# Optimization experiments

Hardware: AMD Instinct MI355X
Metric: run time of the kernel (lower is better)

Reference implementation:

```python
import jax, jax.numpy as jnp
import numpy as np

S, B, E, H = 2048, 64, 256, 256

def setup_inputs() -> dict:
    key = jax.random.key(0)
    k1, k2, k3, k4, k5 = jax.random.split(key, 5)
    scale = 1.0 / np.sqrt(H)
    return {
        "sentence": jax.random.normal(k1, (S, B, E), dtype=jnp.float32),
        "h0": jax.random.uniform(k2, (B, H), dtype=jnp.float32),
        "W_ih": jax.random.normal(k3, (E, H), dtype=jnp.float32) * scale,
        "W_hh": jax.random.normal(k4, (H, H), dtype=jnp.float32) * scale,
        "b": jax.random.normal(k5, (H,), dtype=jnp.float32) * scale,
    }

def reference(sentence, h0, W_ih, W_hh, b):
    # Precompute input projections for all steps in one big GEMM: [S,B,H]
    x_proj = jnp.einsum("sbe,eh->sbh", sentence, W_ih) + b

    def step(h, xp):
        h_new = jnp.tanh(xp + h @ W_hh)  # [B,H]
        return h_new, None

    h_final, _ = jax.lax.scan(step, h0, x_proj)
    return h_final  # [B,H]
```

## Files before the change

kernel.cpp:

```cpp
#include <hip/hip_runtime.h>
#include <math.h>

#define S_TOT 2048
#define B_    64
#define E_    256
#define H_    256

typedef __fp16 half2v __attribute__((ext_vector_type(2)));

__global__ __launch_bounds__(256, 1) void fused_step(
    const float* __restrict__ A,
    const float* __restrict__ Wih,
    const float* __restrict__ bias,
    float*       __restrict__ xp_next,
    const float* __restrict__ xp_cur,
    const float* __restrict__ Whh,
    float*       __restrict__ h,
    int steps, int scan_blocks)
{
    __shared__ float smem[32 * 68 + 32 * 64];
    const int tid = threadIdx.x;

    if ((int)blockIdx.x < scan_blocks) {
        float* hbuf = smem;
        const int b  = blockIdx.x;
        const int ks = tid & 7;
        const int jg = tid >> 3;
        const int j0 = jg << 3;
        const int jf = j0 + ((ks & 1) << 2) + (ks & 2) + ((ks >> 2) & 1);

        half2v w[16][8];
        #pragma unroll
        for (int i = 0; i < 16; i++) {
            const float* r0 = &Whh[(size_t)(ks * 32 + 2 * i) * H_ + j0];
            const float* r1 = r0 + H_;
            #pragma unroll
            for (int jj = 0; jj < 8; jj++) {
                half2v v = __builtin_amdgcn_cvt_pkrtz(r0[jj], r1[jj]);
                int vi = __builtin_bit_cast(int, v);
                asm volatile("" : "+v"(vi));
                w[i][jj] = __builtin_bit_cast(half2v, vi);
            }
        }

        if (tid < 128) {
            half2v hp = __builtin_amdgcn_cvt_pkrtz(h[b * H_ + 2 * tid],
                                                   h[b * H_ + 2 * tid + 1]);
            const int j = 2 * tid;
            ((half2v*)hbuf)[(j >> 5) * 20 + ((j & 31) >> 1)] = hp;
        }
        float xpn = xp_cur[(size_t)b * H_ + jf];
        __syncthreads();

        int p = 0;
        for (int s = 0; s < steps; s++) {
            const float xpc = xpn;
            if (s + 1 < steps)
                xpn = xp_cur[((size_t)(s + 1) * B_ + b) * H_ + jf];

            half2v hk[16];
            {
                const float4* hs = (const float4*)&hbuf[p * 160 + ks * 20];
                float4 t0 = hs[0], t1 = hs[1], t2 = hs[2], t3 = hs[3];
                *(float4*)&hk[0]  = t0;
                *(float4*)&hk[4]  = t1;
                *(float4*)&hk[8]  = t2;
                *(float4*)&hk[12] = t3;
            }

            float acc[8] = {0.f, 0.f, 0.f, 0.f, 0.f, 0.f, 0.f, 0.f};
            #pragma unroll
            for (int i = 0; i < 16; i++) {
                #pragma unroll
                for (int jj = 0; jj < 8; jj++)
                    acc[jj] = __builtin_amdgcn_fdot2(hk[i], w[i][jj],
                                                     acc[jj], false);
            }

            const bool b0 = (ks & 1), b1 = (ks & 2), b2 = (ks & 4);
            float r0, r1, r2, r3, q0, q1, v;
            {
                float s0 = b0 ? acc[0] : acc[4];
                float s1 = b0 ? acc[1] : acc[5];
                float s2 = b0 ? acc[2] : acc[6];
                float s3 = b0 ? acc[3] : acc[7];
                r0 = (b0 ? acc[4] : acc[0]) + __shfl_xor(s0, 1);
                r1 = (b0 ? acc[5] : acc[1]) + __shfl_xor(s1, 1);
                r2 = (b0 ? acc[6] : acc[2]) + __shfl_xor(s2, 1);
                r3 = (b0 ? acc[7] : acc[3]) + __shfl_xor(s3, 1);
            }
            {
                float s0 = b1 ? r0 : r2;
                float s1 = b1 ? r1 : r3;
                q0 = (b1 ? r2 : r0) + __shfl_xor(s0, 2);
                q1 = (b1 ? r3 : r1) + __shfl_xor(s1, 2);
            }
            {
                float s0 = b2 ? q0 : q1;
                v = (b2 ? q1 : q0) + __shfl_xor(s0, 4);
            }

            v += xpc;
            const float e2 = __expf(2.f * v);
            const float hn = 1.f - 2.f / (e2 + 1.f);
            ((__fp16*)hbuf)[((p ^ 1) * 160 + (jf >> 5) * 20) * 2 + (jf & 31)]
                = (__fp16)hn;
            if (s == steps - 1) h[b * H_ + jf] = hn;
            __syncthreads();
            p ^= 1;
        }
    } else if (A != nullptr) {
        float (*As)[68] = (float(*)[68])smem;
        float (*Bs)[64] = (float(*)[64])(smem + 32 * 68);

        const int gid = blockIdx.x - scan_blocks;
        const int bm = (gid >> 2) * 64;
        const int bn = (gid & 3) * 64;
        const int tx = tid & 15;
        const int ty = tid >> 4;

        float acc[4][4] = {};

        const int ar = tid >> 3;
        const int ak = (tid & 7) << 2;
        const int br = tid >> 4;
        const int bc = (tid & 15) << 2;

        for (int k0 = 0; k0 < E_; k0 += 32) {
            float4 a0 = *(const float4*)&A[(size_t)(bm + ar)      * E_ + k0 + ak];
            float4 a1 = *(const float4*)&A[(size_t)(bm + ar + 32) * E_ + k0 + ak];
            float4 bv0 = *(const float4*)&Wih[(size_t)(k0 + br)      * H_ + bn + bc];
            float4 bv1 = *(const float4*)&Wih[(size_t)(k0 + br + 16) * H_ + bn + bc];

            As[ak+0][ar]    = a0.x; As[ak+1][ar]    = a0.y; As[ak+2][ar]    = a0.z; As[ak+3][ar]    = a0.w;
            As[ak+0][ar+32] = a1.x; As[ak+1][ar+32] = a1.y; As[ak+2][ar+32] = a1.z; As[ak+3][ar+32] = a1.w;
            *(float4*)&Bs[br][bc]      = bv0;
            *(float4*)&Bs[br + 16][bc] = bv1;
            __syncthreads();

            #pragma unroll
            for (int kk = 0; kk < 32; kk++) {
                const float4 av = *(const float4*)&As[kk][ty << 2];
                const float4 bv = *(const float4*)&Bs[kk][tx << 2];
                acc[0][0] += av.x*bv.x; acc[0][1] += av.x*bv.y; acc[0][2] += av.x*bv.z; acc[0][3] += av.x*bv.w;
                acc[1][0] += av.y*bv.x; acc[1][1] += av.y*bv.y; acc[1][2] += av.y*bv.z; acc[1][3] += av.y*bv.w;
                acc[2][0] += av.z*bv.x; acc[2][1] += av.z*bv.y; acc[2][2] += av.z*bv.z; acc[2][3] += av.z*bv.w;
                acc[3][0] += av.w*bv.x; acc[3][1] += av.w*bv.y; acc[3][2] += av.w*bv.z; acc[3][3] += av.w*bv.w;
            }
            __syncthreads();
        }

        const float4 bb = *(const float4*)&bias[bn + (tx << 2)];
        #pragma unroll
        for (int i = 0; i < 4; i++) {
            float4 o;
            o.x = acc[i][0] + bb.x;
            o.y = acc[i][1] + bb.y;
            o.z = acc[i][2] + bb.z;
            o.w = acc[i][3] + bb.w;
            *(float4*)&xp_next[(size_t)(bm + (ty << 2) + i) * H_ + bn + (tx << 2)] = o;
        }
    }
}

extern "C" void kernel_launch(void* const* d_in, const int* in_sizes, int n_in,
                              void* d_out, int out_size, void* d_ws, size_t ws_size,
                              hipStream_t stream)
{
    const float* sentence = (const float*)d_in[0];
    const float* h0       = (const float*)d_in[1];
    const float* W_ih     = (const float*)d_in[2];
    const float* W_hh     = (const float*)d_in[3];
    const float* bias     = (const float*)d_in[4];
    float* h  = (float*)d_out;
    float* ws = (float*)d_ws;

    int chunk = 256;
    while ((size_t)2 * chunk * B_ * H_ * sizeof(float) > ws_size && chunk > 32)
        chunk >>= 1;
    const int nchunk = S_TOT / chunk;
    float* buf[2] = { ws, ws + (size_t)chunk * B_ * H_ };

    hipMemcpyAsync(h, h0, B_ * H_ * sizeof(float), hipMemcpyDeviceToDevice, stream);

    fused_step<<<chunk * 4, 256, 0, stream>>>(sentence, W_ih, bias, buf[0],
                                              nullptr, W_hh, h, 0, 0);
    for (int c = 0; c < nchunk; c++) {
        const bool last = (c == nchunk - 1);
        const int gemmb = last ? 0 : chunk * 4;
        const float* Anext = last ? nullptr
                                  : sentence + (size_t)(c + 1) * chunk * B_ * E_;
        fused_step<<<64 + gemmb, 256, 0, stream>>>(Anext, W_ih, bias,
                                                   buf[(c + 1) & 1],
                                                   buf[c & 1], W_hh, h,
                                                   chunk, 64);
    }
}
```

Before: 1.441 ms.

## Double threads per block to halve per-thread recurrent dot work

Blocks grow from 256 to 512 threads. In the recurrent scan, each thread now owns 4 output columns instead of 8, which halves its resident W_hh register slice, its fdot2 chain and the shuffle reduction depth per step. In the projection GEMM, each thread now computes 2 rows instead of 4. The aim is a shorter serial critical path per timestep in the latency-bound scan. The cost is redundant work: half of the lanes compute duplicate results that only one lane writes, and more waves contend for each block barrier.

```diff
diff --git a/kernel.cpp b/kernel.cpp
--- a/kernel.cpp
+++ b/kernel.cpp
@@ -8,7 +8,7 @@
 
 typedef __fp16 half2v __attribute__((ext_vector_type(2)));
 
-__global__ __launch_bounds__(256, 1) void fused_step(
+__global__ __launch_bounds__(512, 2) void fused_step(
     const float* __restrict__ A,
     const float* __restrict__ Wih,
     const float* __restrict__ bias,
@@ -26,16 +26,16 @@
         const int b  = blockIdx.x;
         const int ks = tid & 7;
         const int jg = tid >> 3;
-        const int j0 = jg << 3;
-        const int jf = j0 + ((ks & 1) << 2) + (ks & 2) + ((ks >> 2) & 1);
+        const int j0 = jg << 2;
+        const int jf = j0 + ((ks & 1) << 1) + ((ks >> 1) & 1);
 
-        half2v w[16][8];
+        half2v w[16][4];
         #pragma unroll
         for (int i = 0; i < 16; i++) {
             const float* r0 = &Whh[(size_t)(ks * 32 + 2 * i) * H_ + j0];
             const float* r1 = r0 + H_;
             #pragma unroll
-            for (int jj = 0; jj < 8; jj++) {
+            for (int jj = 0; jj < 4; jj++) {
                 half2v v = __builtin_amdgcn_cvt_pkrtz(r0[jj], r1[jj]);
                 int vi = __builtin_bit_cast(int, v);
                 asm volatile("" : "+v"(vi));
@@ -68,44 +68,37 @@
                 *(float4*)&hk[12] = t3;
             }
 
-            float acc[8] = {0.f, 0.f, 0.f, 0.f, 0.f, 0.f, 0.f, 0.f};
+            float acc[4] = {0.f, 0.f, 0.f, 0.f};
             #pragma unroll
             for (int i = 0; i < 16; i++) {
                 #pragma unroll
-                for (int jj = 0; jj < 8; jj++)
+                for (int jj = 0; jj < 4; jj++)
                     acc[jj] = __builtin_amdgcn_fdot2(hk[i], w[i][jj],
                                                      acc[jj], false);
             }
 
             const bool b0 = (ks & 1), b1 = (ks & 2), b2 = (ks & 4);
-            float r0, r1, r2, r3, q0, q1, v;
+            float r0, r1, q, v;
             {
-                float s0 = b0 ? acc[0] : acc[4];
-                float s1 = b0 ? acc[1] : acc[5];
-                float s2 = b0 ? acc[2] : acc[6];
-                float s3 = b0 ? acc[3] : acc[7];
-                r0 = (b0 ? acc[4] : acc[0]) + __shfl_xor(s0, 1);
-                r1 = (b0 ? acc[5] : acc[1]) + __shfl_xor(s1, 1);
-                r2 = (b0 ? acc[6] : acc[2]) + __shfl_xor(s2, 1);
-                r3 = (b0 ? acc[7] : acc[3]) + __shfl_xor(s3, 1);
+                float s0 = b0 ? acc[0] : acc[2];
+                float s1 = b0 ? acc[1] : acc[3];
+                r0 = (b0 ? acc[2] : acc[0]) + __shfl_xor(s0, 1);
+                r1 = (b0 ? acc[3] : acc[1]) + __shfl_xor(s1, 1);
             }
             {
-                float s0 = b1 ? r0 : r2;
-                float s1 = b1 ? r1 : r3;
-                q0 = (b1 ? r2 : r0) + __shfl_xor(s0, 2);
-                q1 = (b1 ? r3 : r1) + __shfl_xor(s1, 2);
+                float s0 = b1 ? r0 : r1;
+                q = (b1 ? r1 : r0) + __shfl_xor(s0, 2);
             }
-            {
-                float s0 = b2 ? q0 : q1;
-                v = (b2 ? q1 : q0) + __shfl_xor(s0, 4);
-            }
+            v = q + __shfl_xor(q, 4);
 
             v += xpc;
             const float e2 = __expf(2.f * v);
             const float hn = 1.f - 2.f / (e2 + 1.f);
-            ((__fp16*)hbuf)[((p ^ 1) * 160 + (jf >> 5) * 20) * 2 + (jf & 31)]
-                = (__fp16)hn;
-            if (s == steps - 1) h[b * H_ + jf] = hn;
+            if (!b2) {
+                ((__fp16*)hbuf)[(p ^ 1) * 320 + (jf >> 5) * 40 + (jf & 31)]
+                    = (__fp16)hn;
+                if (s == steps - 1) h[b * H_ + jf] = hn;
+            }
             __syncthreads();
             p ^= 1;
         }
@@ -119,7 +112,7 @@
         const int tx = tid & 15;
         const int ty = tid >> 4;
 
-        float acc[4][4] = {};
+        float acc[2][4] = {};
 
         const int ar = tid >> 3;
         const int ak = (tid & 7) << 2;
@@ -127,38 +120,35 @@
         const int bc = (tid & 15) << 2;
 
         for (int k0 = 0; k0 < E_; k0 += 32) {
-            float4 a0 = *(const float4*)&A[(size_t)(bm + ar)      * E_ + k0 + ak];
-            float4 a1 = *(const float4*)&A[(size_t)(bm + ar + 32) * E_ + k0 + ak];
-            float4 bv0 = *(const float4*)&Wih[(size_t)(k0 + br)      * H_ + bn + bc];
-            float4 bv1 = *(const float4*)&Wih[(size_t)(k0 + br + 16) * H_ + bn + bc];
+            float4 a0  = *(const float4*)&A[(size_t)(bm + ar) * E_ + k0 + ak];
+            float4 bv0 = *(const float4*)&Wih[(size_t)(k0 + br) * H_ + bn + bc];
 
-            As[ak+0][ar]    = a0.x; As[ak+1][ar]    = a0.y; As[ak+2][ar]    = a0.z; As[ak+3][ar]    = a0.w;
-            As[ak+0][ar+32] = a1.x; As[ak+1][ar+32] = a1.y; As[ak+2][ar+32] = a1.z; As[ak+3][ar+32] = a1.w;
-            *(float4*)&Bs[br][bc]      = bv0;
-            *(float4*)&Bs[br + 16][bc] = bv1;
+            As[ak+0][ar] = a0.x; As[ak+1][ar] = a0.y;
+            As[ak+2][ar] = a0.z; As[ak+3][ar] = a0.w;
+            *(float4*)&Bs[br][bc] = bv0;
             __syncthreads();
 
             #pragma unroll
             for (int kk = 0; kk < 32; kk++) {
-                const float4 av = *(const float4*)&As[kk][ty << 2];
+                const float2 av = *(const float2*)&As[kk][ty << 1];
                 const float4 bv = *(const float4*)&Bs[kk][tx << 2];
-                acc[0][0] += av.x*bv.x; acc[0][1] += av.x*bv.y; acc[0][2] += av.x*bv.z; acc[0][3] += av.x*bv.w;
-                acc[1][0] += av.y*bv.x; acc[1][1] += av.y*bv.y; acc[1][2] += av.y*bv.z; acc[1][3] += av.y*bv.w;
-                acc[2][0] += av.z*bv.x; acc[2][1] += av.z*bv.y; acc[2][2] += av.z*bv.z; acc[2][3] += av.z*bv.w;
-                acc[3][0] += av.w*bv.x; acc[3][1] += av.w*bv.y; acc[3][2] += av.w*bv.z; acc[3][3] += av.w*bv.w;
+                acc[0][0] += av.x*bv.x; acc[0][1] += av.x*bv.y;
+                acc[0][2] += av.x*bv.z; acc[0][3] += av.x*bv.w;
+                acc[1][0] += av.y*bv.x; acc[1][1] += av.y*bv.y;
+                acc[1][2] += av.y*bv.z; acc[1][3] += av.y*bv.w;
             }
             __syncthreads();
         }
 
         const float4 bb = *(const float4*)&bias[bn + (tx << 2)];
         #pragma unroll
-        for (int i = 0; i < 4; i++) {
+        for (int i = 0; i < 2; i++) {
             float4 o;
             o.x = acc[i][0] + bb.x;
             o.y = acc[i][1] + bb.y;
             o.z = acc[i][2] + bb.z;
             o.w = acc[i][3] + bb.w;
-            *(float4*)&xp_next[(size_t)(bm + (ty << 2) + i) * H_ + bn + (tx << 2)] = o;
+            *(float4*)&xp_next[(size_t)(bm + (ty << 1) + i) * H_ + bn + (tx << 2)] = o;
         }
     }
 }
@@ -183,14 +173,14 @@
 
     hipMemcpyAsync(h, h0, B_ * H_ * sizeof(float), hipMemcpyDeviceToDevice, stream);
 
-    fused_step<<<chunk * 4, 256, 0, stream>>>(sentence, W_ih, bias, buf[0],
+    fused_step<<<chunk * 4, 512, 0, stream>>>(sentence, W_ih, bias, buf[0],
                                               nullptr, W_hh, h, 0, 0);
     for (int c = 0; c < nchunk; c++) {
         const bool last = (c == nchunk - 1);
         const int gemmb = last ? 0 : chunk * 4;
         const float* Anext = last ? nullptr
                                   : sentence + (size_t)(c + 1) * chunk * B_ * E_;
-        fused_step<<<64 + gemmb, 256, 0, stream>>>(Anext, W_ih, bias,
+        fused_step<<<64 + gemmb, 512, 0, stream>>>(Anext, W_ih, bias,
                                                    buf[(c + 1) & 1],
                                                    buf[c & 1], W_hh, h,
                                                    chunk, 64);
```

Result: slower. 1.502 ms (+4.2%).

## Compute recurrent step with MFMA over 16-row batch tiles per block

Applied to the files above, without the earlier changes.

The recurrent scan moves from one block per batch row using fdot2 and shuffle reductions to one block per 16 batch rows using 16x16x32 f16 MFMA. W_hh stays resident in registers as MFMA B fragments. h is exchanged through an XOR-swizzled LDS buffer, written with DPP-packed stores. This removes the cross-lane reduction and cuts the scan to 4 blocks, lowering per-step latency, but only 4 CUs now run the serial chain and register pressure rises.

```diff
diff --git a/kernel.cpp b/kernel.cpp
--- a/kernel.cpp
+++ b/kernel.cpp
@@ -7,8 +7,21 @@
 #define H_    256
 
 typedef __fp16 half2v __attribute__((ext_vector_type(2)));
-
-__global__ __launch_bounds__(256, 1) void fused_step(
+typedef __fp16 half8v __attribute__((ext_vector_type(8)));
+typedef float  f32x4  __attribute__((ext_vector_type(4)));
+
+__device__ __forceinline__ float dpp_xor1(float x) {
+    int i = __builtin_bit_cast(int, x);
+    i = __builtin_amdgcn_mov_dpp(i, 0xB1, 0xF, 0xF, true);
+    return __builtin_bit_cast(float, i);
+}
+__device__ __forceinline__ int dpp_xor2_i(int i) {
+    return __builtin_amdgcn_mov_dpp(i, 0x4E, 0xF, 0xF, true);
+}
+
+__global__ __launch_bounds__(256)
+__attribute__((amdgpu_waves_per_eu(1, 1)))
+void fused_step(
     const float* __restrict__ A,
     const float* __restrict__ Wih,
     const float* __restrict__ bias,
@@ -22,91 +35,150 @@
     const int tid = threadIdx.x;
 
     if ((int)blockIdx.x < scan_blocks) {
-        float* hbuf = smem;
-        const int b  = blockIdx.x;
-        const int ks = tid & 7;
-        const int jg = tid >> 3;
-        const int j0 = jg << 3;
-        const int jf = j0 + ((ks & 1) << 2) + (ks & 2) + ((ks >> 2) & 1);
-
-        half2v w[16][8];
-        #pragma unroll
-        for (int i = 0; i < 16; i++) {
-            const float* r0 = &Whh[(size_t)(ks * 32 + 2 * i) * H_ + j0];
-            const float* r1 = r0 + H_;
-            #pragma unroll
-            for (int jj = 0; jj < 8; jj++) {
-                half2v v = __builtin_amdgcn_cvt_pkrtz(r0[jj], r1[jj]);
-                int vi = __builtin_bit_cast(int, v);
-                asm volatile("" : "+v"(vi));
-                w[i][jj] = __builtin_bit_cast(half2v, vi);
-            }
-        }
-
-        if (tid < 128) {
-            half2v hp = __builtin_amdgcn_cvt_pkrtz(h[b * H_ + 2 * tid],
-                                                   h[b * H_ + 2 * tid + 1]);
-            const int j = 2 * tid;
-            ((half2v*)hbuf)[(j >> 5) * 20 + ((j & 31) >> 1)] = hp;
-        }
-        float xpn = xp_cur[(size_t)b * H_ + jf];
+        char* hb = (char*)smem;
+        const int b0   = blockIdx.x * 16;
+        const int lane = tid & 63;
+        const int wv   = tid >> 6;
+        const int lm   = lane & 15;
+        const int lg   = lane >> 4;
+        const int coln = wv * 64 + lm;
+        const int row0 = lg * 4;
+
+#define DECLWF(kt,jt) half8v wf_##kt##_##jt;
+#define WF_ALL(X) \
+        X(0,0) X(0,1) X(0,2) X(0,3)  X(1,0) X(1,1) X(1,2) X(1,3) \
+        X(2,0) X(2,1) X(2,2) X(2,3)  X(3,0) X(3,1) X(3,2) X(3,3) \
+        X(4,0) X(4,1) X(4,2) X(4,3)  X(5,0) X(5,1) X(5,2) X(5,3) \
+        X(6,0) X(6,1) X(6,2) X(6,3)  X(7,0) X(7,1) X(7,2) X(7,3)
+        WF_ALL(DECLWF)
+
+#define LOADWF(kt,jt) { \
+        const float* p_ = &Whh[(size_t)((kt)*32 + lg*8) * H_ + wv*64 + (jt)*16 + lm]; \
+        int i0_ = __builtin_bit_cast(int, __builtin_amdgcn_cvt_pkrtz(p_[0],     p_[H_])); \
+        int i1_ = __builtin_bit_cast(int, __builtin_amdgcn_cvt_pkrtz(p_[2*H_],  p_[3*H_])); \
+        int i2_ = __builtin_bit_cast(int, __builtin_amdgcn_cvt_pkrtz(p_[4*H_],  p_[5*H_])); \
+        int i3_ = __builtin_bit_cast(int, __builtin_amdgcn_cvt_pkrtz(p_[6*H_],  p_[7*H_])); \
+        asm volatile("" : "+v"(i0_), "+v"(i1_), "+v"(i2_), "+v"(i3_)); \
+        int4 t_; t_.x = i0_; t_.y = i1_; t_.z = i2_; t_.w = i3_; \
+        wf_##kt##_##jt = __builtin_bit_cast(half8v, t_); \
+    }
+        WF_ALL(LOADWF)
+
+        {
+            const int m  = tid >> 4;
+            const int kq = (tid & 15) * 16;
+            const float* src = &h[(size_t)(b0 + m) * H_ + kq];
+            float4 f0 = *(const float4*)(src + 0);
+            float4 f1 = *(const float4*)(src + 4);
+            float4 f2 = *(const float4*)(src + 8);
+            float4 f3 = *(const float4*)(src + 12);
+            int4 u0, u1;
+            u0.x = __builtin_bit_cast(int, __builtin_amdgcn_cvt_pkrtz(f0.x, f0.y));
+            u0.y = __builtin_bit_cast(int, __builtin_amdgcn_cvt_pkrtz(f0.z, f0.w));
+            u0.z = __builtin_bit_cast(int, __builtin_amdgcn_cvt_pkrtz(f1.x, f1.y));
+            u0.w = __builtin_bit_cast(int, __builtin_amdgcn_cvt_pkrtz(f1.z, f1.w));
+            u1.x = __builtin_bit_cast(int, __builtin_amdgcn_cvt_pkrtz(f2.x, f2.y));
+            u1.y = __builtin_bit_cast(int, __builtin_amdgcn_cvt_pkrtz(f2.z, f2.w));
+            u1.z = __builtin_bit_cast(int, __builtin_amdgcn_cvt_pkrtz(f3.x, f3.y));
+            u1.w = __builtin_bit_cast(int, __builtin_amdgcn_cvt_pkrtz(f3.z, f3.w));
+            const int base = m * 512 + kq * 2;
+            *(int4*)(hb + ((base)      ^ ((m & 7) << 4))) = u0;
+            *(int4*)(hb + ((base + 16) ^ ((m & 7) << 4))) = u1;
+        }
+
+        int ro[8];
+        #pragma unroll
+        for (int kt = 0; kt < 8; kt++)
+            ro[kt] = (lm * 512 + kt * 64 + lg * 16) ^ ((lm & 7) << 4);
+        int wo[16];
+        #pragma unroll
+        for (int jt = 0; jt < 4; jt++)
+            #pragma unroll
+            for (int r = 0; r < 4; r++) {
+                const int m = row0 + r, n = coln + jt * 16;
+                wo[jt * 4 + r] = (m * 512 + n * 2) ^ ((m & 7) << 4);
+            }
+        const size_t xcol = (size_t)(b0 + row0) * H_ + coln;
+
+        float xc[16];
+        #pragma unroll
+        for (int jt = 0; jt < 4; jt++)
+            #pragma unroll
+            for (int r = 0; r < 4; r++)
+                xc[jt * 4 + r] = xp_cur[xcol + (size_t)r * H_ + jt * 16];
+
         __syncthreads();
 
         int p = 0;
         for (int s = 0; s < steps; s++) {
-            const float xpc = xpn;
-            if (s + 1 < steps)
-                xpn = xp_cur[((size_t)(s + 1) * B_ + b) * H_ + jf];
-
-            half2v hk[16];
-            {
-                const float4* hs = (const float4*)&hbuf[p * 160 + ks * 20];
-                float4 t0 = hs[0], t1 = hs[1], t2 = hs[2], t3 = hs[3];
-                *(float4*)&hk[0]  = t0;
-                *(float4*)&hk[4]  = t1;
-                *(float4*)&hk[8]  = t2;
-                *(float4*)&hk[12] = t3;
-            }
-
-            float acc[8] = {0.f, 0.f, 0.f, 0.f, 0.f, 0.f, 0.f, 0.f};
+            const char* rb = hb + p * 8192;
+            char*       wb = hb + (p ^ 1) * 8192;
+
+#define LOADAF(kt) half8v af##kt = __builtin_bit_cast(half8v, *(const float4*)(rb + ro[kt]));
+            LOADAF(0) LOADAF(1) LOADAF(2) LOADAF(3)
+            LOADAF(4) LOADAF(5) LOADAF(6) LOADAF(7)
+
+            float xn[16];
+            if (s + 1 < steps) {
+                const size_t xb = (size_t)(s + 1) * B_ * H_ + xcol;
+                #pragma unroll
+                for (int jt = 0; jt < 4; jt++)
+                    #pragma unroll
+                    for (int r = 0; r < 4; r++)
+                        xn[jt * 4 + r] = xp_cur[xb + (size_t)r * H_ + jt * 16];
+            }
+
+            f32x4 c0 = {0.f,0.f,0.f,0.f}, c1 = {0.f,0.f,0.f,0.f};
+            f32x4 c2 = {0.f,0.f,0.f,0.f}, c3 = {0.f,0.f,0.f,0.f};
+#define MFJT(jt) \
+            c##jt = __builtin_amdgcn_mfma_f32_16x16x32_f16(af0, wf_0_##jt, c##jt, 0,0,0); \
+            c##jt = __builtin_amdgcn_mfma_f32_16x16x32_f16(af1, wf_1_##jt, c##jt, 0,0,0); \
+            c##jt = __builtin_amdgcn_mfma_f32_16x16x32_f16(af2, wf_2_##jt, c##jt, 0,0,0); \
+            c##jt = __builtin_amdgcn_mfma_f32_16x16x32_f16(af3, wf_3_##jt, c##jt, 0,0,0); \
+            c##jt = __builtin_amdgcn_mfma_f32_16x16x32_f16(af4, wf_4_##jt, c##jt, 0,0,0); \
+            c##jt = __builtin_amdgcn_mfma_f32_16x16x32_f16(af5, wf_5_##jt, c##jt, 0,0,0); \
+            c##jt = __builtin_amdgcn_mfma_f32_16x16x32_f16(af6, wf_6_##jt, c##jt, 0,0,0); \
+            c##jt = __builtin_amdgcn_mfma_f32_16x16x32_f16(af7, wf_7_##jt, c##jt, 0,0,0);
+            MFJT(0) MFJT(1) MFJT(2) MFJT(3)
+
+            float hv[16];
+#define FIN(jt, r) { \
+            float v_  = c##jt[r] + xc[(jt)*4 + (r)]; \
+            float e2_ = __expf(2.f * v_); \
+            hv[(jt)*4 + (r)] = 1.f - 2.f / (e2_ + 1.f); \
+        }
+            FIN(0,0) FIN(0,1) FIN(0,2) FIN(0,3)
+            FIN(1,0) FIN(1,1) FIN(1,2) FIN(1,3)
+            FIN(2,0) FIN(2,1) FIN(2,2) FIN(2,3)
+            FIN(3,0) FIN(3,1) FIN(3,2) FIN(3,3)
+            if (s == steps - 1) {
+                #pragma unroll
+                for (int jt = 0; jt < 4; jt++)
+                    #pragma unroll
+                    for (int r = 0; r < 4; r++)
+                        h[xcol + (size_t)r * H_ + jt * 16] = hv[jt * 4 + r];
+            }
+
+            int pkA[16], pkB[16];
             #pragma unroll
             for (int i = 0; i < 16; i++) {
+                float o1 = dpp_xor1(hv[i]);
+                pkA[i] = __builtin_bit_cast(int, __builtin_amdgcn_cvt_pkrtz(hv[i], o1));
+                pkB[i] = dpp_xor2_i(pkA[i]);
+            }
+            if ((lane & 3) == 0) {
                 #pragma unroll
-                for (int jj = 0; jj < 8; jj++)
-                    acc[jj] = __builtin_amdgcn_fdot2(hk[i], w[i][jj],
-                                                     acc[jj], false);
-            }
-
-            const bool b0 = (ks & 1), b1 = (ks & 2), b2 = (ks & 4);
-            float r0, r1, r2, r3, q0, q1, v;
-            {
-                float s0 = b0 ? acc[0] : acc[4];
-                float s1 = b0 ? acc[1] : acc[5];
-                float s2 = b0 ? acc[2] : acc[6];
-                float s3 = b0 ? acc[3] : acc[7];
-                r0 = (b0 ? acc[4] : acc[0]) + __shfl_xor(s0, 1);
-                r1 = (b0 ? acc[5] : acc[1]) + __shfl_xor(s1, 1);
-                r2 = (b0 ? acc[6] : acc[2]) + __shfl_xor(s2, 1);
-                r3 = (b0 ? acc[7] : acc[3]) + __shfl_xor(s3, 1);
-            }
-            {
-                float s0 = b1 ? r0 : r2;
-                float s1 = b1 ? r1 : r3;
-                q0 = (b1 ? r2 : r0) + __shfl_xor(s0, 2);
-                q1 = (b1 ? r3 : r1) + __shfl_xor(s1, 2);
-            }
-            {
-                float s0 = b2 ? q0 : q1;
-                v = (b2 ? q1 : q0) + __shfl_xor(s0, 4);
-            }
-
-            v += xpc;
-            const float e2 = __expf(2.f * v);
-            const float hn = 1.f - 2.f / (e2 + 1.f);
-            ((__fp16*)hbuf)[((p ^ 1) * 160 + (jf >> 5) * 20) * 2 + (jf & 31)]
-                = (__fp16)hn;
-            if (s == steps - 1) h[b * H_ + jf] = hn;
-            __syncthreads();
+                for (int i = 0; i < 16; i++) {
+                    int2 w2; w2.x = pkA[i]; w2.y = pkB[i];
+                    *(int2*)(wb + wo[i]) = w2;
+                }
+            }
+
+            #pragma unroll
+            for (int i = 0; i < 16; i++) xc[i] = xn[i];
+
+            asm volatile("s_waitcnt lgkmcnt(0)" ::: "memory");
+            __builtin_amdgcn_s_barrier();
             p ^= 1;
         }
     } else if (A != nullptr) {
@@ -181,7 +253,7 @@
     const int nchunk = S_TOT / chunk;
     float* buf[2] = { ws, ws + (size_t)chunk * B_ * H_ };
 
-    hipMemcpyAsync(h, h0, B_ * H_ * sizeof(float), hipMemcpyDeviceToDevice, stream);
+    (void)hipMemcpyAsync(h, h0, B_ * H_ * sizeof(float), hipMemcpyDeviceToDevice, stream);
 
     fused_step<<<chunk * 4, 256, 0, stream>>>(sentence, W_ih, bias, buf[0],
                                               nullptr, W_hh, h, 0, 0);
@@ -190,9 +262,9 @@
         const int gemmb = last ? 0 : chunk * 4;
         const float* Anext = last ? nullptr
                                   : sentence + (size_t)(c + 1) * chunk * B_ * E_;
-        fused_step<<<64 + gemmb, 256, 0, stream>>>(Anext, W_ih, bias,
-                                                   buf[(c + 1) & 1],
-                                                   buf[c & 1], W_hh, h,
-                                                   chunk, 64);
+        fused_step<<<4 + gemmb, 256, 0, stream>>>(Anext, W_ih, bias,
+                                                  buf[(c + 1) & 1],
+                                                  buf[c & 1], W_hh, h,
+                                                  chunk, 4);
     }
 }
```

After: 3.263 ms. +126.5%, slower.
